# Optimization experiments

Measured on AMD Instinct MI355X. Metric: run time of the kernel, lower is better.

The kernel has to match this reference:

```python
import jax, jax.numpy as jnp
import numpy as np
import math

HIDDEN = 1024
HEADS = 16
HEAD_DIM = HIDDEN // HEADS


def setup_inputs() -> dict:
    key = jax.random.key(0)
    ks = jax.random.split(key, 9)
    s = 1.0 / math.sqrt(HIDDEN)
    return {
        "x": jax.random.normal(ks[0], (4, 2048, HIDDEN), dtype=jnp.float32),
        "Wq": jax.random.normal(ks[1], (HIDDEN, HIDDEN), dtype=jnp.float32) * s,
        "bq": jnp.zeros((HIDDEN,), dtype=jnp.float32),
        "Wk": jax.random.normal(ks[2], (HIDDEN, HIDDEN), dtype=jnp.float32) * s,
        "bk": jnp.zeros((HIDDEN,), dtype=jnp.float32),
        "Wv": jax.random.normal(ks[3], (HIDDEN, HIDDEN), dtype=jnp.float32) * s,
        "bv": jnp.zeros((HIDDEN,), dtype=jnp.float32),
        "Wo": jax.random.normal(ks[4], (HIDDEN, HIDDEN), dtype=jnp.float32) * s,
        "bo": jnp.zeros((HIDDEN,), dtype=jnp.float32),
    }


def reference(x, Wq, bq, Wk, bk, Wv, bv, Wo, bo):
    B, L, D = x.shape
    H, hd = HEADS, HEAD_DIM
    # QKV projections (weights stored as [in, out], i.e. torch W.T)
    q = (x @ Wq + bq).reshape(B, L, H, hd).transpose(0, 2, 1, 3)  # [B,H,L,hd]
    k = (x @ Wk + bk).reshape(B, L, H, hd).transpose(0, 2, 1, 3)
    v = (x @ Wv + bv).reshape(B, L, H, hd).transpose(0, 2, 1, 3)
    scores = jnp.einsum("bhqd,bhkd->bhqk", q, k) / math.sqrt(hd)  # [B,H,L,L]
    causal_mask = jnp.triu(jnp.full((L, L), -jnp.inf, dtype=scores.dtype), k=1)
    att = jax.nn.softmax(scores + causal_mask, axis=-1)
    out = jnp.einsum("bhqk,bhkd->bhqd", att, v)  # [B,H,L,hd]
    out = out.transpose(0, 2, 1, 3).reshape(B, L, D)
    return out @ Wo + bo
```

## Files before the change

### kernel.cpp

```cpp
#include <hip/hip_runtime.h>
#include <stdint.h>

#define LOG2E 1.44269504088896340736f

typedef __attribute__((ext_vector_type(8))) short short8;
typedef __attribute__((ext_vector_type(4))) float float4v;
typedef __attribute__((ext_vector_type(4))) unsigned int uint4v;
typedef __attribute__((ext_vector_type(2))) unsigned int uint2v;

typedef const __attribute__((address_space(1))) unsigned int gu32;
typedef __attribute__((address_space(3))) unsigned int lu32;

__device__ __forceinline__ void async16(const unsigned short* g, unsigned short* l){
  __builtin_amdgcn_global_load_lds((gu32*)g, (lu32*)l, 16, 0, 0);
}

__device__ __forceinline__ unsigned short f2bf(float f){
  union { float f; unsigned int u; } v; v.f = f;
  unsigned int u = v.u;
  return (unsigned short)((u + 0x7FFFu + ((u >> 16) & 1u)) >> 16);
}
__device__ __forceinline__ unsigned int pkbf(float a, float b){
  unsigned int r;
  asm("v_cvt_pk_bf16_f32 %0, %1, %2" : "=v"(r) : "v"(a), "v"(b));
  return r;
}

__device__ __forceinline__ void pl32(unsigned int &a, unsigned int &b){
#if __has_builtin(__builtin_amdgcn_permlane32_swap)
  uint2v r = __builtin_amdgcn_permlane32_swap(a, b, false, false);
  a = r[0]; b = r[1];
#else
  asm("v_permlane32_swap_b32 %0, %1" : "+v"(a), "+v"(b));
#endif
}
__device__ __forceinline__ void pl16(unsigned int &a, unsigned int &b){
#if __has_builtin(__builtin_amdgcn_permlane16_swap)
  uint2v r = __builtin_amdgcn_permlane16_swap(a, b, false, false);
  a = r[0]; b = r[1];
#else
  asm("v_permlane16_swap_b32 %0, %1" : "+v"(a), "+v"(b));
#endif
}

__global__ void prelude_kernel(const float* __restrict__ x, unsigned short* __restrict__ xb,
                               const float* __restrict__ Wq, const float* __restrict__ Wk,
                               const float* __restrict__ Wv, const float* __restrict__ Wo,
                               unsigned short* __restrict__ wqkvT, unsigned short* __restrict__ woT){
  __shared__ float tileS[64][68];
  const int bid = blockIdx.x;
  if (bid < 4096){
    int t = bid * 256 + threadIdx.x;
    const float4v* xp = (const float4v*)x;
    float4v a = xp[2*t], b = xp[2*t+1];
    short8 o;
    o[0]=(short)f2bf(a[0]); o[1]=(short)f2bf(a[1]); o[2]=(short)f2bf(a[2]); o[3]=(short)f2bf(a[3]);
    o[4]=(short)f2bf(b[0]); o[5]=(short)f2bf(b[1]); o[6]=(short)f2bf(b[2]); o[7]=(short)f2bf(b[3]);
    ((short8*)xb)[t] = o;
    return;
  }
  const int wid = bid - 4096;
  int mat = wid >> 8, tile = wid & 255;
  int tk = tile >> 4, tn = tile & 15;
  const float* W = (mat==0)?Wq:(mat==1)?Wk:(mat==2)?Wv:Wo;
  int k0 = tk*64, n0 = tn*64;
  int tid = threadIdx.x;
  #pragma unroll
  for (int it=0; it<4; ++it){
    int idx = tid + it*256;
    int r = idx >> 4, c4 = idx & 15;
    float4v v = *(const float4v*)&W[(uint64_t)(k0+r)*1024 + n0 + c4*4];
    tileS[r][c4*4+0]=v[0]; tileS[r][c4*4+1]=v[1]; tileS[r][c4*4+2]=v[2]; tileS[r][c4*4+3]=v[3];
  }
  __syncthreads();
  unsigned short* dst; int nbase;
  if (mat<3){ dst = wqkvT; nbase = mat*1024 + n0; } else { dst = woT; nbase = n0; }
  #pragma unroll
  for (int it=0; it<2; ++it){
    int idx = tid + it*256;
    int n = idx >> 3, g = idx & 7;
    short8 o;
    #pragma unroll
    for (int j=0;j<8;++j) o[j] = (short)f2bf(tileS[g*8+j][n]);
    *(short8*)&dst[(uint64_t)(nbase+n)*1024 + k0 + g*8] = o;
  }
}

__global__ __launch_bounds__(512, 2) void gemm_qkv_kernel(
    const unsigned short* __restrict__ A, const unsigned short* __restrict__ BT,
    const float* __restrict__ bias0, const float* __restrict__ bias1, const float* __restrict__ bias2,
    unsigned short* __restrict__ oq, unsigned short* __restrict__ ok,
    unsigned short* __restrict__ ov)
{
  __shared__ __attribute__((aligned(16))) unsigned short lsAll[65536];
  const int tid = threadIdx.x, lane = tid & 63, wave = tid >> 6;
  const int wr = wave >> 2, wc = wave & 3;
  const int id = blockIdx.x;
  const int by = id & 31, bx = id >> 5;
  const int m0 = by * 256, n0 = bx * 256;
  const int c = lane & 15, quad = lane >> 4;
  const float QSCALE = 0.125f * LOG2E;

  float4v acc[8][4];
  #pragma unroll
  for (int i=0;i<8;++i)
    #pragma unroll
    for (int j=0;j<4;++j) acc[i][j] = (float4v){0.f,0.f,0.f,0.f};

  auto STAGE = [&](int kt2, int bufc){
    #pragma unroll
    for (int l=0;l<4;++l){
      int gl = l*512 + tid;
      int row = gl >> 3, gp = gl & 7, gs = gp ^ (row & 7);
      async16(&A[(uint64_t)(m0+row)*1024 + kt2*64 + gs*8], &lsAll[bufc*16384 + gl*8]);
    }
    #pragma unroll
    for (int l=0;l<4;++l){
      int gl = l*512 + tid;
      int row = gl >> 3, gp = gl & 7, gs = gp ^ (row & 7);
      async16(&BT[(uint64_t)(n0+row)*1024 + kt2*64 + gs*8], &lsAll[32768 + bufc*16384 + gl*8]);
    }
  };

  STAGE(0, 0);
  STAGE(1, 1);
  asm volatile("s_waitcnt vmcnt(8)" ::: "memory");
  __builtin_amdgcn_s_barrier();

  for (int kt = 0; kt < 16; ++kt){
    const int cur = kt & 1;
    const unsigned short* lA = &lsAll[cur*16384];
    const unsigned short* lB = &lsAll[32768 + cur*16384];
    #pragma unroll
    for (int kk=0; kk<2; ++kk){
      short8 bf[4], af[4];
      #pragma unroll
      for (int j=0;j<4;++j){
        int row = wc*64 + j*16 + c;
        int g = (kk*4 + quad) ^ (row & 7);
        bf[j] = *(const short8*)&lB[row*64 + g*8];
      }
      #pragma unroll
      for (int i4=0;i4<4;++i4){
        int row = wr*128 + i4*16 + c;
        int g = (kk*4 + quad) ^ (row & 7);
        af[i4] = *(const short8*)&lA[row*64 + g*8];
      }
      #pragma unroll
      for (int i4=0;i4<4;++i4)
        #pragma unroll
        for (int j=0;j<4;++j)
          acc[i4][j] = __builtin_amdgcn_mfma_f32_16x16x32_bf16(af[i4], bf[j], acc[i4][j], 0, 0, 0);
      #pragma unroll
      for (int i4=0;i4<4;++i4){
        int row = wr*128 + 64 + i4*16 + c;
        int g = (kk*4 + quad) ^ (row & 7);
        af[i4] = *(const short8*)&lA[row*64 + g*8];
      }
      #pragma unroll
      for (int i4=0;i4<4;++i4)
        #pragma unroll
        for (int j=0;j<4;++j)
          acc[4+i4][j] = __builtin_amdgcn_mfma_f32_16x16x32_bf16(af[i4], bf[j], acc[4+i4][j], 0, 0, 0);
    }
    if (kt < 15){
      __builtin_amdgcn_s_barrier();
      if (kt < 14){
        STAGE(kt+2, cur);
        asm volatile("s_waitcnt vmcnt(8)" ::: "memory");
      } else {
        asm volatile("s_waitcnt vmcnt(0)" ::: "memory");
      }
      __builtin_amdgcn_s_barrier();
    }
  }

  const int sel = bx >> 2;
  const int n0l = (bx & 3) * 256;
  const int h0 = n0l >> 6;
  const int bb = m0 >> 11, l0 = m0 & 2047;
  const float* bp = (sel==0)?bias0:(sel==1)?bias1:bias2;
  float bj[4];
  #pragma unroll
  for (int j=0;j<4;++j) bj[j] = bp[n0l + wc*64 + j*16 + c];
  __syncthreads();
  unsigned short* lE = lsAll;
  if (sel < 2){
    unsigned short* dst = (sel==0)?oq:ok;
    #pragma unroll
    for (int i=0;i<8;++i){
      #pragma unroll
      for (int r=0;r<4;++r){
        int row = wr*128 + i*16 + quad*4 + r;
        #pragma unroll
        for (int j=0;j<4;++j){
          float v = acc[i][j][r] + bj[j];
          if (sel == 0) v *= QSCALE;
          int col = wc*64 + j*16 + c;
          int gg = col >> 3;
          int gsw = (gg & 24) | ((gg & 7) ^ (row & 7));
          lE[row*256 + gsw*8 + (col & 7)] = f2bf(v);
        }
      }
    }
    __syncthreads();
    #pragma unroll
    for (int it=0; it<16; ++it){
      int gl = it*512 + tid;
      int row = gl >> 5, gg = gl & 31;
      int gsw = (gg & 24) | ((gg & 7) ^ (row & 7));
      short8 w = *(const short8*)&lE[row*256 + gsw*8];
      int hh = h0 + (gg >> 3);
      *(short8*)&dst[((uint64_t)(bb*16 + hh)*2048 + l0 + row)*64 + (gg & 7)*8] = w;
    }
  } else {
    #pragma unroll
    for (int i=0;i<8;++i){
      #pragma unroll
      for (int r=0;r<4;++r){
        int mloc = wr*128 + i*16 + quad*4 + r;
        int mgg = mloc >> 3;
        #pragma unroll
        for (int j=0;j<4;++j){
          float v = acc[i][j][r] + bj[j];
          int col = wc*64 + j*16 + c;
          int gsT = (mgg & 24) | ((mgg & 7) ^ (col & 7));
          lE[col*256 + gsT*8 + (mloc & 7)] = f2bf(v);
        }
      }
    }
    __syncthreads();
    #pragma unroll
    for (int it=0; it<16; ++it){
      int idx = it*512 + tid;
      int mg = idx & 31, cc = idx >> 5;
      int gsT2 = (mg & 24) | ((mg & 7) ^ (cc & 7));
      short8 w = *(const short8*)&lE[cc*256 + gsT2*8];
      int hh = h0 + (cc >> 6), d = cc & 63;
      *(short8*)&ov[((uint64_t)(bb*16 + hh)*64 + d)*2048 + l0 + mg*8] = w;
    }
  }
}

__global__ __launch_bounds__(256, 3) void gemm_out_kernel(
    const unsigned short* __restrict__ A, const unsigned short* __restrict__ BT,
    const float* __restrict__ bias0, float* __restrict__ of)
{
  __shared__ __attribute__((aligned(16))) unsigned short lS[2*128*64];
  unsigned short* lA = lS;
  unsigned short* lB = lS + 128*64;
  const int tid = threadIdx.x, lane = tid & 63, wave = tid >> 6;
  const int wr = wave >> 1, wc = wave & 1;
  const int by = blockIdx.x & 63, bx = blockIdx.x >> 6;
  const int m0 = by * 128, n0 = bx * 128;
  const int c = lane & 15, quad = lane >> 4;

  float4v acc[4][4];
  #pragma unroll
  for (int i=0;i<4;++i)
    #pragma unroll
    for (int j=0;j<4;++j) acc[i][j] = (float4v){0.f,0.f,0.f,0.f};

  for (int kt = 0; kt < 16; ++kt){
    __syncthreads();
    #pragma unroll
    for (int it=0; it<4; ++it){
      int gl = (wave*4+it)*64 + lane;
      int row = gl >> 3, gp = gl & 7, gs = gp ^ (row & 7);
      async16(&A[(uint64_t)(m0+row)*1024 + kt*64 + gs*8], &lA[gl*8]);
    }
    #pragma unroll
    for (int it=0; it<4; ++it){
      int gl = (wave*4+it)*64 + lane;
      int row = gl >> 3, gp = gl & 7, gs = gp ^ (row & 7);
      async16(&BT[(uint64_t)(n0+row)*1024 + kt*64 + gs*8], &lB[gl*8]);
    }
    __syncthreads();
    #pragma unroll
    for (int kk=0; kk<2; ++kk){
      short8 af[4], bf[4];
      #pragma unroll
      for (int i=0;i<4;++i){
        int row = wr*64 + i*16 + c;
        int g = (quad + kk*4) ^ (row & 7);
        af[i] = *(const short8*)&lA[row*64 + g*8];
      }
      #pragma unroll
      for (int j=0;j<4;++j){
        int row = wc*64 + j*16 + c;
        int g = (quad + kk*4) ^ (row & 7);
        bf[j] = *(const short8*)&lB[row*64 + g*8];
      }
      #pragma unroll
      for (int i=0;i<4;++i)
        #pragma unroll
        for (int j=0;j<4;++j)
          acc[i][j] = __builtin_amdgcn_mfma_f32_16x16x32_bf16(af[i], bf[j], acc[i][j], 0, 0, 0);
    }
  }

  float* lf = (float*)lS;
  float bj[4];
  #pragma unroll
  for (int j=0;j<4;++j) bj[j] = bias0[n0 + wc*64 + j*16 + c];
  #pragma unroll
  for (int half=0; half<2; ++half){
    __syncthreads();
    if (wr == half){
      #pragma unroll
      for (int i=0;i<4;++i){
        #pragma unroll
        for (int r=0;r<4;++r){
          int lrow = i*16 + quad*4 + r;
          #pragma unroll
          for (int j=0;j<4;++j){
            int col = wc*64 + j*16 + c;
            int gg = col >> 2;
            int gs2 = (gg & 24) | ((gg & 7) ^ (lrow & 7));
            lf[lrow*128 + gs2*4 + (col & 3)] = acc[i][j][r] + bj[j];
          }
        }
      }
    }
    __syncthreads();
    #pragma unroll
    for (int it=0; it<8; ++it){
      int gl = it*256 + tid;
      int lrow = gl >> 5, gg = gl & 31;
      int gs2 = (gg & 24) | ((gg & 7) ^ (lrow & 7));
      float4v w = *(const float4v*)&lf[lrow*128 + gs2*4];
      *(float4v*)&of[(uint64_t)(m0 + half*64 + lrow)*1024 + n0 + gg*4] = w;
    }
  }
}

__global__ __launch_bounds__(256, 3) void attn_kernel(
    const unsigned short* __restrict__ q, const unsigned short* __restrict__ k,
    const unsigned short* __restrict__ vt, unsigned short* __restrict__ o)
{
  __shared__ __attribute__((aligned(16))) unsigned short lK[2][64*64];
  __shared__ __attribute__((aligned(16))) unsigned short lV[2][64*64];

  const int idx = blockIdx.x;
  const int bh = idx & 63;
  const int g4 = idx >> 8;
  const int u4 = (idx >> 6) & 3;
  const int qt = (g4==0) ? (15 - u4) : (g4==1) ? (8 + u4) : (g4==2) ? (7 - u4) : u4;
  const int tid = threadIdx.x, lane = tid & 63, wave = tid >> 6;
  const int c = lane & 15, quad = lane >> 4;

  const unsigned short* qh = q  + (uint64_t)bh * (2048*64);
  const unsigned short* kh = k  + (uint64_t)bh * (2048*64);
  const unsigned short* vh = vt + (uint64_t)bh * (64*2048);

  short8 qf[2][2];
  #pragma unroll
  for (int u=0;u<2;++u)
    #pragma unroll
    for (int kk=0;kk<2;++kk){
      int row = qt*128 + u*64 + wave*16 + c;
      qf[u][kk] = *(const short8*)&qh[(uint64_t)row*64 + (kk*4+quad)*8];
    }

  #pragma unroll
  for (int it=0; it<2; ++it){
    int gl = (wave*2+it)*64 + lane;
    int row = gl >> 3, gp = gl & 7, gs = gp ^ (row & 7);
    async16(&kh[(uint64_t)row*64 + gs*8], &lK[0][gl*8]);
    async16(&vh[(uint64_t)row*2048 + gs*8], &lV[0][gl*8]);
  }

  const float4v z4 = {0.f,0.f,0.f,0.f};
  const uint4v onesu = {0x3F803F80u,0x3F803F80u,0x3F803F80u,0x3F803F80u};
  const short8 ones8 = __builtin_bit_cast(short8, onesu);

  float4v accO[2][4];
  #pragma unroll
  for (int u=0;u<2;++u)
    #pragma unroll
    for (int t=0;t<4;++t) accO[u][t] = z4;
  float4v accL4[2];
  accL4[0] = z4; accL4[1] = z4;

  const int ktEnd = 2*qt + 1;

  for (int kt = 0; kt <= ktEnd; ++kt){
    __syncthreads();
    const int cb = kt & 1;

    if (kt < ktEnd){
      const int nb = 1 - cb;
      #pragma unroll
      for (int it=0; it<2; ++it){
        int gl = (wave*2+it)*64 + lane;
        int row = gl >> 3, gp = gl & 7, gs = gp ^ (row & 7);
        async16(&kh[(uint64_t)((kt+1)*64 + row)*64 + gs*8], &lK[nb][gl*8]);
        async16(&vh[(uint64_t)row*2048 + (kt+1)*64 + gs*8], &lV[nb][gl*8]);
      }
    }

    const bool doU0  = (kt != ktEnd);
    const bool lastT = (kt == ktEnd);
    const bool diag0 = doU0 && (kt == 2*qt);

    float4v s[2][4];
    #pragma unroll
    for (int kk=0; kk<2; ++kk){
      short8 kf[4];
      #pragma unroll
      for (int j=0;j<4;++j){
        if (lastT && j > wave) continue;
        int row = j*16 + c;
        int g = (kk*4 + quad) ^ (row & 7);
        kf[j] = *(const short8*)&lK[cb][row*64 + g*8];
      }
      __builtin_amdgcn_s_setprio(1);
      #pragma unroll
      for (int j=0;j<4;++j){
        if (lastT && j > wave) continue;
        s[1][j] = __builtin_amdgcn_mfma_f32_16x16x32_bf16(kf[j], qf[1][kk],
                    (kk==0)? z4 : s[1][j], 0, 0, 0);
      }
      if (doU0){
        #pragma unroll
        for (int j=0;j<4;++j){
          if (diag0 && j > wave) continue;
          s[0][j] = __builtin_amdgcn_mfma_f32_16x16x32_bf16(kf[j], qf[0][kk],
                      (kk==0)? z4 : s[0][j], 0, 0, 0);
        }
      }
      __builtin_amdgcn_s_setprio(0);
    }

    short8 pa[2][2];
    #pragma unroll
    for (int u=1;u>=0;--u){
      if (u==0 && !doU0) continue;
      const bool isDiagU = (u==1) ? lastT : diag0;
      const int qb_u = qt*128 + u*64 + wave*16;
      const bool needMask = (kt*64 + 63 > qb_u);
      const int qg = qb_u + c;
      unsigned int w[4][2];
      #pragma unroll
      for (int j=0;j<4;++j){
        if (isDiagU && j > wave){ w[j][0]=0u; w[j][1]=0u; continue; }
        float p0,p1,p2,p3;
        {
          float4v sv = s[u][j];
          p0 = __builtin_amdgcn_exp2f(sv[0]);
          p1 = __builtin_amdgcn_exp2f(sv[1]);
          p2 = __builtin_amdgcn_exp2f(sv[2]);
          p3 = __builtin_amdgcn_exp2f(sv[3]);
        }
        if (needMask){
          int keyb = kt*64 + j*16 + quad*4;
          if (keyb + 0 > qg) p0 = 0.f;
          if (keyb + 1 > qg) p1 = 0.f;
          if (keyb + 2 > qg) p2 = 0.f;
          if (keyb + 3 > qg) p3 = 0.f;
        }
        w[j][0] = pkbf(p0,p1);
        w[j][1] = pkbf(p2,p3);
      }
      #pragma unroll
      for (int kk=0;kk<2;++kk){
        if (isDiagU && kk==1 && wave < 2) continue;
        unsigned int a0 = w[2*kk+0][0], b0 = w[2*kk+1][0];
        unsigned int a1 = w[2*kk+0][1], b1 = w[2*kk+1][1];
        pl32(a0,b0); pl32(a1,b1);
        pl16(a0,b0); pl16(a1,b1);
        uint4v uv; uv[0]=a0; uv[1]=a1; uv[2]=b0; uv[3]=b1;
        pa[u][kk] = __builtin_bit_cast(short8, uv);
      }
    }

    #pragma unroll
    for (int kk=0; kk<2; ++kk){
      const bool needU1 = !(lastT && kk==1 && wave < 2);
      const bool needU0 = doU0 && !(diag0 && kk==1 && wave < 2);
      short8 bv[4];
      if (needU1 || needU0){
        #pragma unroll
        for (int t=0;t<4;++t){
          int row = t*16 + c;
          int g = (kk*4 + quad) ^ (row & 7);
          bv[t] = *(const short8*)&lV[cb][row*64 + g*8];
        }
      }
      __builtin_amdgcn_s_setprio(1);
      if (needU1){
        #pragma unroll
        for (int t=0;t<4;++t)
          accO[1][t] = __builtin_amdgcn_mfma_f32_16x16x32_bf16(pa[1][kk], bv[t], accO[1][t], 0, 0, 0);
        accL4[1] = __builtin_amdgcn_mfma_f32_16x16x32_bf16(pa[1][kk], ones8, accL4[1], 0, 0, 0);
      }
      if (needU0){
        #pragma unroll
        for (int t=0;t<4;++t)
          accO[0][t] = __builtin_amdgcn_mfma_f32_16x16x32_bf16(pa[0][kk], bv[t], accO[0][t], 0, 0, 0);
        accL4[0] = __builtin_amdgcn_mfma_f32_16x16x32_bf16(pa[0][kk], ones8, accL4[0], 0, 0, 0);
      }
      __builtin_amdgcn_s_setprio(0);
    }
  }

  __syncthreads();

  const int b = bh >> 4, h = bh & 15;
  unsigned short* lPf = &lK[0][0];
  #pragma unroll
  for (int u=0;u<2;++u){
    #pragma unroll
    for (int r=0;r<4;++r){
      float rinv = 1.0f / accL4[u][r];
      int mloc = u*64 + wave*16 + quad*4 + r;
      #pragma unroll
      for (int t=0;t<4;++t){
        int col = t*16 + c;
        int gg = col >> 3;
        int gs2 = gg ^ (mloc & 7);
        lPf[mloc*64 + gs2*8 + (col & 7)] = f2bf(accO[u][t][r] * rinv);
      }
    }
  }
  __syncthreads();
  #pragma unroll
  for (int it=0; it<4; ++it){
    int gl = it*256 + tid;
    int row = gl >> 3, gg = gl & 7;
    int gs2 = gg ^ (row & 7);
    short8 w = *(const short8*)&lPf[row*64 + gs2*8];
    uint64_t m = (uint64_t)b*2048 + qt*128 + row;
    *(short8*)&o[m*1024 + h*64 + gg*8] = w;
  }
}

extern "C" void kernel_launch(void* const* d_in, const int* in_sizes, int n_in,
                              void* d_out, int out_size, void* d_ws, size_t ws_size,
                              hipStream_t stream)
{
  (void)in_sizes; (void)n_in; (void)out_size; (void)ws_size;
  const float* x  = (const float*)d_in[0];
  const float* Wq = (const float*)d_in[1];
  const float* bq = (const float*)d_in[2];
  const float* Wk = (const float*)d_in[3];
  const float* bk = (const float*)d_in[4];
  const float* Wv = (const float*)d_in[5];
  const float* bv = (const float*)d_in[6];
  const float* Wo = (const float*)d_in[7];
  const float* bo = (const float*)d_in[8];
  float* out = (float*)d_out;

  char* ws = (char*)d_ws;
  unsigned short* xb    = (unsigned short*)(ws);
  unsigned short* wqkvT = (unsigned short*)(ws + (16ull<<20));
  unsigned short* woT   = (unsigned short*)(ws + (22ull<<20));
  unsigned short* qb    = (unsigned short*)(ws + (24ull<<20));
  unsigned short* kb    = (unsigned short*)(ws + (40ull<<20));
  unsigned short* vtb   = (unsigned short*)(ws + (56ull<<20));
  unsigned short* ab    = xb;

  prelude_kernel<<<5120, 256, 0, stream>>>(x, xb, Wq, Wk, Wv, Wo, wqkvT, woT);
  gemm_qkv_kernel<<<384, 512, 0, stream>>>(xb, wqkvT, bq, bk, bv, qb, kb, vtb);
  attn_kernel<<<1024, 256, 0, stream>>>(qb, kb, vtb, ab);
  gemm_out_kernel<<<512, 256, 0, stream>>>(ab, woT, bo, out);
}
```

Before: 238.8 us.

## Interleave half-tile global prefetch with MFMA phases in QKV GEMM main loop

Restructures the QKV projection GEMM main loop into an 8-phase ping-pong schedule. Global-to-LDS prefetches are split into half-tile chunks issued between LDS fragment loads and MFMA groups, with explicit barriers, sched_barriers and s_setprio raised around the MFMA blocks. The goal is to overlap memory traffic with matrix math more finely than the old stage-then-compute loop, which stalled on barriers. In exchange it adds many more workgroup barriers and a fragile hand-tuned vmcnt accounting that must match the exact order of the loads.

```diff
diff --git a/kernel.cpp b/kernel.cpp
--- a/kernel.cpp
+++ b/kernel.cpp
@@ -107,72 +107,105 @@
     #pragma unroll
     for (int j=0;j<4;++j) acc[i][j] = (float4v){0.f,0.f,0.f,0.f};
 
-  auto STAGE = [&](int kt2, int bufc){
-    #pragma unroll
-    for (int l=0;l<4;++l){
-      int gl = l*512 + tid;
-      int row = gl >> 3, gp = gl & 7, gs = gp ^ (row & 7);
-      async16(&A[(uint64_t)(m0+row)*1024 + kt2*64 + gs*8], &lsAll[bufc*16384 + gl*8]);
-    }
-    #pragma unroll
-    for (int l=0;l<4;++l){
-      int gl = l*512 + tid;
-      int row = gl >> 3, gp = gl & 7, gs = gp ^ (row & 7);
-      async16(&BT[(uint64_t)(n0+row)*1024 + kt2*64 + gs*8], &lsAll[32768 + bufc*16384 + gl*8]);
+  auto STAGEH = [&](int mat, int kt2, int buf, int half){
+    const unsigned short* src = mat ? BT : A;
+    const int base0 = mat ? 32768 : 0;
+    const uint64_t rb = mat ? (uint64_t)n0 : (uint64_t)m0;
+    #pragma unroll
+    for (int l=0;l<2;++l){
+      int fgl = half*1024 + l*512 + tid;
+      int row = fgl >> 3, gp = fgl & 7, gs = gp ^ (row & 7);
+      async16(&src[(rb+row)*1024 + kt2*64 + gs*8], &lsAll[base0 + buf*16384 + fgl*8]);
     }
   };
 
-  STAGE(0, 0);
-  STAGE(1, 1);
-  asm volatile("s_waitcnt vmcnt(8)" ::: "memory");
+  short8 af[4], bf[4];
+  auto LOADB = [&](int buf, int kk){
+    #pragma unroll
+    for (int j=0;j<4;++j){
+      int row = wc*64 + j*16 + c;
+      int g = (kk*4 + quad) ^ (row & 7);
+      bf[j] = *(const short8*)&lsAll[32768 + buf*16384 + row*64 + g*8];
+    }
+  };
+  auto LOADA = [&](int buf, int kk, int mh){
+    #pragma unroll
+    for (int i4=0;i4<4;++i4){
+      int row = wr*128 + mh*64 + i4*16 + c;
+      int g = (kk*4 + quad) ^ (row & 7);
+      af[i4] = *(const short8*)&lsAll[buf*16384 + row*64 + g*8];
+    }
+  };
+  auto MFMAQ = [&](int mh){
+    __builtin_amdgcn_s_setprio(1);
+    #pragma unroll
+    for (int i4=0;i4<4;++i4)
+      #pragma unroll
+      for (int j=0;j<4;++j)
+        acc[mh*4+i4][j] = __builtin_amdgcn_mfma_f32_16x16x32_bf16(af[i4], bf[j], acc[mh*4+i4][j], 0, 0, 0);
+    __builtin_amdgcn_s_setprio(0);
+  };
+
+  #pragma unroll
+  for (int h=0;h<2;++h){ STAGEH(0,0,0,h); STAGEH(1,0,0,h); }
+  STAGEH(1,1,1,0);
+  asm volatile("s_waitcnt vmcnt(2)" ::: "memory");
   __builtin_amdgcn_s_barrier();
 
-  for (int kt = 0; kt < 16; ++kt){
-    const int cur = kt & 1;
-    const unsigned short* lA = &lsAll[cur*16384];
-    const unsigned short* lB = &lsAll[32768 + cur*16384];
-    #pragma unroll
-    for (int kk=0; kk<2; ++kk){
-      short8 bf[4], af[4];
-      #pragma unroll
-      for (int j=0;j<4;++j){
-        int row = wc*64 + j*16 + c;
-        int g = (kk*4 + quad) ^ (row & 7);
-        bf[j] = *(const short8*)&lB[row*64 + g*8];
-      }
-      #pragma unroll
-      for (int i4=0;i4<4;++i4){
-        int row = wr*128 + i4*16 + c;
-        int g = (kk*4 + quad) ^ (row & 7);
-        af[i4] = *(const short8*)&lA[row*64 + g*8];
-      }
-      #pragma unroll
-      for (int i4=0;i4<4;++i4)
-        #pragma unroll
-        for (int j=0;j<4;++j)
-          acc[i4][j] = __builtin_amdgcn_mfma_f32_16x16x32_bf16(af[i4], bf[j], acc[i4][j], 0, 0, 0);
-      #pragma unroll
-      for (int i4=0;i4<4;++i4){
-        int row = wr*128 + 64 + i4*16 + c;
-        int g = (kk*4 + quad) ^ (row & 7);
-        af[i4] = *(const short8*)&lA[row*64 + g*8];
-      }
-      #pragma unroll
-      for (int i4=0;i4<4;++i4)
-        #pragma unroll
-        for (int j=0;j<4;++j)
-          acc[4+i4][j] = __builtin_amdgcn_mfma_f32_16x16x32_bf16(af[i4], bf[j], acc[4+i4][j], 0, 0, 0);
-    }
-    if (kt < 15){
-      __builtin_amdgcn_s_barrier();
-      if (kt < 14){
-        STAGE(kt+2, cur);
-        asm volatile("s_waitcnt vmcnt(8)" ::: "memory");
-      } else {
-        asm volatile("s_waitcnt vmcnt(0)" ::: "memory");
-      }
-      __builtin_amdgcn_s_barrier();
-    }
+  for (int i=0; i<8; ++i){
+    const int t1 = 2*i+1, t2 = 2*i+2, t3 = 2*i+3;
+    const bool pf = (i < 7);
+    LOADB(0,0); LOADA(0,0,0); STAGEH(1, t1, 1, 1);
+    __builtin_amdgcn_s_barrier();
+    asm volatile("s_waitcnt lgkmcnt(0)" ::: "memory");
+    __builtin_amdgcn_sched_barrier(0);
+    MFMAQ(0);
+    __builtin_amdgcn_s_barrier();
+    LOADA(0,0,1); STAGEH(0, t1, 1, 0);
+    __builtin_amdgcn_s_barrier();
+    asm volatile("s_waitcnt lgkmcnt(0)" ::: "memory");
+    __builtin_amdgcn_sched_barrier(0);
+    MFMAQ(1);
+    __builtin_amdgcn_s_barrier();
+    LOADB(0,1); LOADA(0,1,0); STAGEH(0, t1, 1, 1);
+    __builtin_amdgcn_s_barrier();
+    asm volatile("s_waitcnt lgkmcnt(0)" ::: "memory");
+    __builtin_amdgcn_sched_barrier(0);
+    MFMAQ(0);
+    __builtin_amdgcn_s_barrier();
+    LOADA(0,1,1); if (pf) STAGEH(1, t2, 0, 0);
+    __builtin_amdgcn_s_barrier();
+    asm volatile("s_waitcnt lgkmcnt(0)" ::: "memory");
+    __builtin_amdgcn_sched_barrier(0);
+    MFMAQ(1);
+    if (pf) asm volatile("s_waitcnt vmcnt(2)" ::: "memory");
+    else    asm volatile("s_waitcnt vmcnt(0)" ::: "memory");
+    __builtin_amdgcn_s_barrier();
+    LOADB(1,0); LOADA(1,0,0); if (pf) STAGEH(1, t2, 0, 1);
+    __builtin_amdgcn_s_barrier();
+    asm volatile("s_waitcnt lgkmcnt(0)" ::: "memory");
+    __builtin_amdgcn_sched_barrier(0);
+    MFMAQ(0);
+    __builtin_amdgcn_s_barrier();
+    LOADA(1,0,1); if (pf) STAGEH(0, t2, 0, 0);
+    __builtin_amdgcn_s_barrier();
+    asm volatile("s_waitcnt lgkmcnt(0)" ::: "memory");
+    __builtin_amdgcn_sched_barrier(0);
+    MFMAQ(1);
+    __builtin_amdgcn_s_barrier();
+    LOADB(1,1); LOADA(1,1,0); if (pf) STAGEH(0, t2, 0, 1);
+    __builtin_amdgcn_s_barrier();
+    asm volatile("s_waitcnt lgkmcnt(0)" ::: "memory");
+    __builtin_amdgcn_sched_barrier(0);
+    MFMAQ(0);
+    __builtin_amdgcn_s_barrier();
+    LOADA(1,1,1); if (pf) STAGEH(1, t3, 1, 0);
+    __builtin_amdgcn_s_barrier();
+    asm volatile("s_waitcnt lgkmcnt(0)" ::: "memory");
+    __builtin_amdgcn_sched_barrier(0);
+    MFMAQ(1);
+    if (pf) asm volatile("s_waitcnt vmcnt(2)" ::: "memory");
+    __builtin_amdgcn_s_barrier();
   }
 
   const int sel = bx >> 2;
```

New measurement: 237.7 us. No clear change (-0.4%).
